# Kernel tuning notes

Measured on AMD Instinct MI355X. Metric: run time of the kernel, lower is better.

Reference implementation:

```python
import jax, jax.numpy as jnp
import numpy as np
from jax import lax

K_SIZE = 3
STRIDE = 1
PAD = 1
BN_EPS = 1e-5


def _unfold(x, k, stride, pad):
    # x: [B, C, H, W] -> patches [B, L, C*k*k] with torch.unfold feature
    # ordering (channel-major: feat = c*k*k + i*k + j), L = oH*oW
    B, C, H, W = x.shape
    xp = jnp.pad(x, ((0, 0), (0, 0), (pad, pad), (pad, pad)))
    oH = (H + 2 * pad - k) // stride + 1
    oW = (W + 2 * pad - k) // stride + 1
    views = []
    for i in range(k):
        for j in range(k):
            views.append(xp[:, :, i:i + oH * stride:stride, j:j + oW * stride:stride])
    p = jnp.stack(views, axis=0)            # [k*k, B, C, oH, oW]
    p = p.transpose(1, 3, 4, 2, 0)          # [B, oH, oW, C, k*k]
    return p.reshape(B, oH * oW, C * k * k), oH, oW


def _nearest_l1(flat, cents):
    # Online nearest-centroid search under L1, avoids [N, K] x D blowup.
    # flat: [N, D], cents: [K, D] -> int32 indices [N] (first min on ties,
    # matching torch argmin)
    N = flat.shape[0]
    init = (jnp.full((N,), jnp.inf, flat.dtype), jnp.zeros((N,), jnp.int32))
    ks = jnp.arange(cents.shape[0], dtype=jnp.int32)

    def body(carry, kc):
        kidx, c = kc
        d = jnp.abs(flat - c).sum(-1)       # [N]
        bd, bi = carry
        better = d < bd
        return (jnp.where(better, d, bd), jnp.where(better, kidx, bi)), None

    (_, best_idx), _ = lax.scan(body, init, (ks, cents))
    return best_idx


def setup_inputs() -> dict:
    key = jax.random.key(0)
    ks = jax.random.split(key, 5)
    B, Cin, H, W = 8, 64, 56, 56
    K, D, Cout = 256, Cin * K_SIZE * K_SIZE, 128
    return {
        "x": jax.random.normal(ks[0], (B, Cin, H, W), jnp.float32),
        "centroids": jax.random.normal(ks[1], (K, D), jnp.float32),
        "residual_centroids": jax.random.normal(ks[2], (K, D), jnp.float32),
        "dot_centroids": jax.random.normal(ks[3], (K, Cout), jnp.float32),
        "dot_residual_centroids": jax.random.normal(ks[4], (K, Cout), jnp.float32),
        "bn_gamma": jnp.ones((Cout,), jnp.float32),
        "bn_beta": jnp.zeros((Cout,), jnp.float32),
    }


def reference(x, centroids, residual_centroids, dot_centroids,
              dot_residual_centroids, bn_gamma, bn_beta):
    B = x.shape[0]
    Cout = dot_centroids.shape[1]
    patches, oH, oW = _unfold(x, K_SIZE, STRIDE, PAD)   # [B, L, D]
    L, D = patches.shape[1], patches.shape[2]
    flat = patches.reshape(B * L, D)

    # Stage 1: nearest centroid (L1)
    idx1 = _nearest_l1(flat, centroids)                  # [B*L]
    residuals = flat - centroids[idx1]                   # [B*L, D]
    # Stage 2: nearest residual centroid (L1)
    idx2 = _nearest_l1(residuals, residual_centroids)    # [B*L]

    # LUT gather + sum
    out_vals = dot_centroids[idx1] + dot_residual_centroids[idx2]  # [B*L, Cout]
    out = out_vals.reshape(B, L, Cout).transpose(0, 2, 1).reshape(B, Cout, oH, oW)

    # BatchNorm2d (training mode: biased batch statistics)
    mean = out.mean(axis=(0, 2, 3), keepdims=True)
    var = ((out - mean) ** 2).mean(axis=(0, 2, 3), keepdims=True)
    out = (out - mean) * lax.rsqrt(var + BN_EPS)
    out = out * bn_gamma[None, :, None, None] + bn_beta[None, :, None, None]
    return out
```

## Files before the change

### kernel.cpp

```cpp
#include <hip/hip_runtime.h>

#define NP 25088
#define DD 576
#define KC 256

__global__ __launch_bounds__(256) void unfold_kernel(const float* __restrict__ x,
                                                     float* __restrict__ PT) {
  const int d = blockIdx.y;
  const int n = blockIdx.x * 256 + threadIdx.x;
  const int c = d / 9, r = d % 9;
  const int di = r / 3 - 1, dj = r % 3 - 1;
  const int b = n / 3136, hw = n % 3136;
  const int h = hw / 56 + di, w = hw % 56 + dj;
  float v = 0.0f;
  if (h >= 0 && h < 56 && w >= 0 && w < 56)
    v = x[(((size_t)b * 64 + c) * 56 + h) * 56 + w];
  PT[(size_t)d * NP + n] = v;
}

__global__ __launch_bounds__(256) void transpose_kernel(const float* __restrict__ C,
                                                        float* __restrict__ CT) {
  const int d = blockIdx.x;
  const int k = threadIdx.x;
  CT[d * KC + k] = C[k * DD + d];
}

#define ACC4(p, a, s) \
  do { p.x += fabsf(a.x - (s)); p.y += fabsf(a.y - (s)); \
       p.z += fabsf(a.z - (s)); p.w += fabsf(a.w - (s)); } while (0)
#define ADD4(t, p) \
  do { t.x += p.x; t.y += p.y; t.z += p.z; t.w += p.w; } while (0)
#define COMP(v, i) ((i) == 0 ? (v).x : (i) == 1 ? (v).y : (i) == 2 ? (v).z : (v).w)

__global__ __launch_bounds__(256, 6) void nearest_kernel(const float* __restrict__ AT,
                                                         const float* __restrict__ CT,
                                                         float* __restrict__ distc,
                                                         int* __restrict__ idxc) {
  __shared__ float As[2][16][64];
  __shared__ float Bs[2][16][64];

  const int tid = threadIdx.x;
  const int tm = tid >> 4;
  const int tk = tid & 15;
  const int L = blockIdx.x;
  const int xcd = L & 7, r = L >> 3;
  const int mb = xcd * 49 + (r >> 2);
  const int kc = r & 3;
  const int m0 = mb * 64, k0 = kc * 64;

  float4 ra0, rb0;
  float4 p0, p1, p2, p3, t0, t1, t2, t3;

  const int frow = tid >> 4, fcol = (tid & 15) * 4;
  const float* ap = AT + (size_t)frow * NP + m0 + fcol;
  const float* bp = CT + (size_t)frow * KC + k0 + fcol;

#define LOADT() do {                                       \
    ra0 = *(const float4*)(ap);                            \
    rb0 = *(const float4*)(bp);                            \
    ap += (size_t)16 * NP; bp += 16 * KC;                  \
  } while (0)

#define WRITET(bf) do {                                    \
    *(float4*)&As[bf][frow][fcol] = ra0;                   \
    *(float4*)&Bs[bf][frow][fcol] = rb0;                   \
  } while (0)

  LOADT();
  WRITET(0);
  t0 = t1 = t2 = t3 = make_float4(0.f, 0.f, 0.f, 0.f);

  for (int ch = 0; ch < 36; ++ch) {
    if ((ch & 3) == 0) p0 = p1 = p2 = p3 = make_float4(0.f, 0.f, 0.f, 0.f);
    __syncthreads();
    if (ch < 35) LOADT();
    const float (*__restrict__ Asb)[64] = As[ch & 1];
    const float (*__restrict__ Bsb)[64] = Bs[ch & 1];
#pragma unroll 8
    for (int d = 0; d < 16; ++d) {
      const float4 a = *(const float4*)&Asb[d][tm * 4];
      const float4 b = *(const float4*)&Bsb[d][tk * 4];
      ACC4(p0, a, b.x);
      ACC4(p1, a, b.y);
      ACC4(p2, a, b.z);
      ACC4(p3, a, b.w);
    }
    if (ch < 35) WRITET((ch + 1) & 1);
    if ((ch & 3) == 3) {
      ADD4(t0, p0); ADD4(t1, p1); ADD4(t2, p2); ADD4(t3, p3);
    }
  }

#pragma unroll
  for (int i = 0; i < 4; ++i) {
    const float d0 = COMP(t0, i), d1 = COMP(t1, i), d2 = COMP(t2, i), d3 = COMP(t3, i);
    float bd = d0;
    int bk = k0 + tk * 4;
    if (d1 < bd) { bd = d1; bk = k0 + tk * 4 + 1; }
    if (d2 < bd) { bd = d2; bk = k0 + tk * 4 + 2; }
    if (d3 < bd) { bd = d3; bk = k0 + tk * 4 + 3; }
#pragma unroll
    for (int off = 1; off < 16; off <<= 1) {
      const float od = __shfl_xor(bd, off, 64);
      const int ok = __shfl_xor(bk, off, 64);
      if (od < bd || (od == bd && ok < bk)) { bd = od; bk = ok; }
    }
    if (tk == 0) {
      const int m = m0 + tm * 4 + i;
      distc[(size_t)kc * NP + m] = bd;
      idxc[(size_t)kc * NP + m] = bk;
    }
  }
#undef LOADT
#undef WRITET
}

__global__ __launch_bounds__(256) void combine_kernel(const float* __restrict__ distc,
                                                      const int* __restrict__ idxc,
                                                      int* __restrict__ idx_out) {
  const int n = blockIdx.x * 256 + threadIdx.x;
  if (n >= NP) return;
  float bd = distc[n];
  int bi = idxc[n];
#pragma unroll
  for (int s = 1; s < 4; ++s) {
    const float d = distc[(size_t)s * NP + n];
    if (d < bd) { bd = d; bi = idxc[(size_t)s * NP + n]; }
  }
  idx_out[n] = bi;
}

__global__ __launch_bounds__(256) void resid_kernel(float* __restrict__ PT,
                                                    const float* __restrict__ C1T,
                                                    const int* __restrict__ idx1) {
  const int d = blockIdx.y;
  const int n = blockIdx.x * 256 + threadIdx.x;
  const int k = idx1[n];
  PT[(size_t)d * NP + n] -= C1T[d * KC + k];
}

__global__ __launch_bounds__(256) void stats_kernel(const int* __restrict__ idx1,
                                                    const int* __restrict__ idx2,
                                                    const float* __restrict__ dotc,
                                                    const float* __restrict__ dotrc,
                                                    float* __restrict__ gsum,
                                                    float* __restrict__ gsq) {
  __shared__ float ssum[4][128], ssq[4][128];
  const int tid = threadIdx.x, lane = tid & 63, wv = tid >> 6;
  const int wid = blockIdx.x * 4 + wv;
  float s0 = 0.f, s1 = 0.f, q0 = 0.f, q1 = 0.f;
  for (int n = wid; n < NP; n += 512) {
    const int k1 = idx1[n], k2 = idx2[n];
    const float2 u = ((const float2*)(dotc + (size_t)k1 * 128))[lane];
    const float2 v = ((const float2*)(dotrc + (size_t)k2 * 128))[lane];
    const float x0 = u.x + v.x, x1 = u.y + v.y;
    s0 += x0; s1 += x1; q0 += x0 * x0; q1 += x1 * x1;
  }
  ssum[wv][lane * 2] = s0; ssum[wv][lane * 2 + 1] = s1;
  ssq[wv][lane * 2] = q0;  ssq[wv][lane * 2 + 1] = q1;
  __syncthreads();
  if (tid < 128) {
    const float s = ssum[0][tid] + ssum[1][tid] + ssum[2][tid] + ssum[3][tid];
    const float q = ssq[0][tid] + ssq[1][tid] + ssq[2][tid] + ssq[3][tid];
    atomicAdd(&gsum[tid], s);
    atomicAdd(&gsq[tid], q);
  }
}

__global__ void finalize_kernel(const float* __restrict__ gsum,
                                const float* __restrict__ gsq,
                                const float* __restrict__ gamma,
                                const float* __restrict__ beta,
                                float* __restrict__ scalev,
                                float* __restrict__ shiftv) {
  const int c = threadIdx.x;
  const float mean = gsum[c] * (1.0f / NP);
  const float var = gsq[c] * (1.0f / NP) - mean * mean;
  const float inv = rsqrtf(var + 1e-5f);
  const float sc = gamma[c] * inv;
  scalev[c] = sc;
  shiftv[c] = beta[c] - mean * sc;
}

__global__ __launch_bounds__(256) void output_kernel(const int* __restrict__ idx1,
                                                     const int* __restrict__ idx2,
                                                     const float* __restrict__ dotc,
                                                     const float* __restrict__ dotrc,
                                                     const float* __restrict__ scalev,
                                                     const float* __restrict__ shiftv,
                                                     float* __restrict__ out) {
  __shared__ float vals[64][128];
  const int tid = threadIdx.x, lane = tid & 63, wv = tid >> 6;
  const int blk = blockIdx.x;
  const int b = blk / 49, hw0 = (blk % 49) * 64;
  const int n0 = b * 3136 + hw0;
  const float sc0 = scalev[lane * 2], sc1 = scalev[lane * 2 + 1];
  const float sh0 = shiftv[lane * 2], sh1 = shiftv[lane * 2 + 1];
  for (int t = 0; t < 16; ++t) {
    const int nn = wv * 16 + t;
    const int n = n0 + nn;
    const int k1 = idx1[n], k2 = idx2[n];
    const float2 u = ((const float2*)(dotc + (size_t)k1 * 128))[lane];
    const float2 v = ((const float2*)(dotrc + (size_t)k2 * 128))[lane];
    *(float2*)&vals[nn][lane * 2] =
        make_float2(sc0 * (u.x + v.x) + sh0, sc1 * (u.y + v.y) + sh1);
  }
  __syncthreads();
  const int c = tid >> 1, half = tid & 1;
  float* op = out + ((size_t)b * 128 + c) * 3136 + hw0 + half * 32;
#pragma unroll
  for (int i = 0; i < 32; i += 4) {
    float4 w4;
    w4.x = vals[half * 32 + i + 0][c];
    w4.y = vals[half * 32 + i + 1][c];
    w4.z = vals[half * 32 + i + 2][c];
    w4.w = vals[half * 32 + i + 3][c];
    *(float4*)(op + i) = w4;
  }
}

extern "C" void kernel_launch(void* const* d_in, const int* in_sizes, int n_in,
                              void* d_out, int out_size, void* d_ws, size_t ws_size,
                              hipStream_t stream) {
  const float* x     = (const float*)d_in[0];
  const float* cent  = (const float*)d_in[1];
  const float* rcent = (const float*)d_in[2];
  const float* dotc  = (const float*)d_in[3];
  const float* dotrc = (const float*)d_in[4];
  const float* gamma = (const float*)d_in[5];
  const float* beta  = (const float*)d_in[6];
  float* out = (float*)d_out;

  float* PT  = (float*)d_ws;
  float* C1T = PT + (size_t)DD * NP;
  float* C2T = C1T + (size_t)DD * KC;
  int* idx1  = (int*)(C2T + (size_t)DD * KC);
  int* idx2  = idx1 + NP;
  float* distc = (float*)(idx2 + NP);
  int* idxc    = (int*)(distc + 4 * NP);
  float* gsum   = (float*)(idxc + 4 * NP);
  float* gsq    = gsum + 128;
  float* scalev = gsq + 128;
  float* shiftv = scalev + 128;

  unfold_kernel<<<dim3(98, 576), 256, 0, stream>>>(x, PT);
  transpose_kernel<<<576, 256, 0, stream>>>(cent, C1T);
  transpose_kernel<<<576, 256, 0, stream>>>(rcent, C2T);
  nearest_kernel<<<1568, 256, 0, stream>>>(PT, C1T, distc, idxc);
  combine_kernel<<<98, 256, 0, stream>>>(distc, idxc, idx1);
  resid_kernel<<<dim3(98, 576), 256, 0, stream>>>(PT, C1T, idx1);
  nearest_kernel<<<1568, 256, 0, stream>>>(PT, C2T, distc, idxc);
  combine_kernel<<<98, 256, 0, stream>>>(distc, idxc, idx2);
  hipMemsetAsync(gsum, 0, 256 * sizeof(float), stream);
  stats_kernel<<<128, 256, 0, stream>>>(idx1, idx2, dotc, dotrc, gsum, gsq);
  finalize_kernel<<<1, 128, 0, stream>>>(gsum, gsq, gamma, beta, scalev, shiftv);
  output_kernel<<<392, 256, 0, stream>>>(idx1, idx2, dotc, dotrc, scalev, shiftv, out);
}
```

Measured before the change: 679.4 us.

## Stage nearest-kernel tiles via direct global-to-LDS loads with deeper K chunks

The L1 nearest-centroid kernel now fills its double-buffered shared tiles with direct global-to-LDS buffer loads instead of loading into registers and storing to LDS. The per-stage depth doubles from 16 to 32 feature rows, halving the number of barriers, and the occupancy hint drops from 6 to 5 blocks per CU to fit the larger LDS footprint. This aims to save VGPRs and LDS-store instructions and to overlap the next stage's loads with compute. The risk is that the wait on the asynchronous loads before the barrier is placed correctly, and that lower occupancy hides latency less well.

```diff
diff --git a/kernel.cpp b/kernel.cpp
--- a/kernel.cpp
+++ b/kernel.cpp
@@ -1,4 +1,5 @@
 #include <hip/hip_runtime.h>
+#include <stdint.h>
 
 #define NP 25088
 #define DD 576
@@ -32,14 +33,21 @@
   do { t.x += p.x; t.y += p.y; t.z += p.z; t.w += p.w; } while (0)
 #define COMP(v, i) ((i) == 0 ? (v).x : (i) == 1 ? (v).y : (i) == 2 ? (v).z : (v).w)
 
-__global__ __launch_bounds__(256, 6) void nearest_kernel(const float* __restrict__ AT,
+__device__ __forceinline__ void gl16(const float* g, float* l) {
+  __builtin_amdgcn_global_load_lds(
+      (const __attribute__((address_space(1))) void*)(uintptr_t)g,
+      (__attribute__((address_space(3))) void*)(uintptr_t)l, 16, 0, 0);
+}
+
+__global__ __launch_bounds__(256, 5) void nearest_kernel(const float* __restrict__ AT,
                                                          const float* __restrict__ CT,
                                                          float* __restrict__ distc,
                                                          int* __restrict__ idxc) {
-  __shared__ float As[2][16][64];
-  __shared__ float Bs[2][16][64];
+  __shared__ __align__(16) float As[2][32][64];
+  __shared__ __align__(16) float Bs[2][32][64];
 
   const int tid = threadIdx.x;
+  const int lane = tid & 63, wv = tid >> 6;
   const int tm = tid >> 4;
   const int tk = tid & 15;
   const int L = blockIdx.x;
@@ -48,36 +56,31 @@
   const int kc = r & 3;
   const int m0 = mb * 64, k0 = kc * 64;
 
-  float4 ra0, rb0;
+  const int lr = lane >> 4, lc = (lane & 15) * 4;
+  const float* apg = AT + (size_t)(wv * 8 + lr) * NP + m0 + lc;
+  const float* bpg = CT + (size_t)(wv * 8 + lr) * KC + k0 + lc;
+
+#define STAGE(bf) do {                                     \
+    gl16(apg,              &As[bf][wv * 8][0]);            \
+    gl16(apg + 4 * NP,     &As[bf][wv * 8 + 4][0]);        \
+    gl16(bpg,              &Bs[bf][wv * 8][0]);            \
+    gl16(bpg + 4 * KC,     &Bs[bf][wv * 8 + 4][0]);        \
+    apg += (size_t)32 * NP; bpg += 32 * KC;                \
+  } while (0)
+
   float4 p0, p1, p2, p3, t0, t1, t2, t3;
 
-  const int frow = tid >> 4, fcol = (tid & 15) * 4;
-  const float* ap = AT + (size_t)frow * NP + m0 + fcol;
-  const float* bp = CT + (size_t)frow * KC + k0 + fcol;
-
-#define LOADT() do {                                       \
-    ra0 = *(const float4*)(ap);                            \
-    rb0 = *(const float4*)(bp);                            \
-    ap += (size_t)16 * NP; bp += 16 * KC;                  \
-  } while (0)
-
-#define WRITET(bf) do {                                    \
-    *(float4*)&As[bf][frow][fcol] = ra0;                   \
-    *(float4*)&Bs[bf][frow][fcol] = rb0;                   \
-  } while (0)
-
-  LOADT();
-  WRITET(0);
+  STAGE(0);
   t0 = t1 = t2 = t3 = make_float4(0.f, 0.f, 0.f, 0.f);
-
-  for (int ch = 0; ch < 36; ++ch) {
-    if ((ch & 3) == 0) p0 = p1 = p2 = p3 = make_float4(0.f, 0.f, 0.f, 0.f);
-    __syncthreads();
-    if (ch < 35) LOADT();
+  __syncthreads();
+
+  for (int ch = 0; ch < 18; ++ch) {
+    if ((ch & 1) == 0) p0 = p1 = p2 = p3 = make_float4(0.f, 0.f, 0.f, 0.f);
+    if (ch < 17) STAGE((ch + 1) & 1);
     const float (*__restrict__ Asb)[64] = As[ch & 1];
     const float (*__restrict__ Bsb)[64] = Bs[ch & 1];
 #pragma unroll 8
-    for (int d = 0; d < 16; ++d) {
+    for (int d = 0; d < 32; ++d) {
       const float4 a = *(const float4*)&Asb[d][tm * 4];
       const float4 b = *(const float4*)&Bsb[d][tk * 4];
       ACC4(p0, a, b.x);
@@ -85,10 +88,10 @@
       ACC4(p2, a, b.z);
       ACC4(p3, a, b.w);
     }
-    if (ch < 35) WRITET((ch + 1) & 1);
-    if ((ch & 3) == 3) {
+    if (ch & 1) {
       ADD4(t0, p0); ADD4(t1, p1); ADD4(t2, p2); ADD4(t3, p3);
     }
+    __syncthreads();
   }
 
 #pragma unroll
@@ -111,8 +114,7 @@
       idxc[(size_t)kc * NP + m] = bk;
     }
   }
-#undef LOADT
-#undef WRITET
+#undef STAGE
 }
 
 __global__ __launch_bounds__(256) void combine_kernel(const float* __restrict__ distc,
```

Result: slower. 708.8 us (+4.3%).

## Restructure L1 nearest search: one thread per centroid over row-major patches

Applied to the files above, without the earlier changes.

Patches are now stored row-major ([N, D]) rather than transposed. The nearest-centroid kernel assigns one centroid per thread and 16 points per block, with the point data read at block-uniform addresses so they can be served by scalar loads. The partial-K split, the combine kernels and the centroid transposes are removed, and the residual kernel becomes vectorized by row. The trade-off is that LDS tiling is dropped: every block re-reads the full centroid matrix through cache using strided per-thread rows, which raises L2 traffic and weakens coalescing.

```diff
diff --git a/kernel.cpp b/kernel.cpp
--- a/kernel.cpp
+++ b/kernel.cpp
@@ -1,142 +1,120 @@
 #include <hip/hip_runtime.h>
+#include <stdint.h>
 
 #define NP 25088
 #define DD 576
 #define KC 256
 
 __global__ __launch_bounds__(256) void unfold_kernel(const float* __restrict__ x,
-                                                     float* __restrict__ PT) {
-  const int d = blockIdx.y;
-  const int n = blockIdx.x * 256 + threadIdx.x;
-  const int c = d / 9, r = d % 9;
-  const int di = r / 3 - 1, dj = r % 3 - 1;
-  const int b = n / 3136, hw = n % 3136;
-  const int h = hw / 56 + di, w = hw % 56 + dj;
-  float v = 0.0f;
-  if (h >= 0 && h < 56 && w >= 0 && w < 56)
-    v = x[(((size_t)b * 64 + c) * 56 + h) * 56 + w];
-  PT[(size_t)d * NP + n] = v;
-}
-
-__global__ __launch_bounds__(256) void transpose_kernel(const float* __restrict__ C,
-                                                        float* __restrict__ CT) {
-  const int d = blockIdx.x;
-  const int k = threadIdx.x;
-  CT[d * KC + k] = C[k * DD + d];
-}
-
-#define ACC4(p, a, s) \
-  do { p.x += fabsf(a.x - (s)); p.y += fabsf(a.y - (s)); \
-       p.z += fabsf(a.z - (s)); p.w += fabsf(a.w - (s)); } while (0)
-#define ADD4(t, p) \
-  do { t.x += p.x; t.y += p.y; t.z += p.z; t.w += p.w; } while (0)
-#define COMP(v, i) ((i) == 0 ? (v).x : (i) == 1 ? (v).y : (i) == 2 ? (v).z : (v).w)
-
-__global__ __launch_bounds__(256, 6) void nearest_kernel(const float* __restrict__ AT,
-                                                         const float* __restrict__ CT,
-                                                         float* __restrict__ distc,
-                                                         int* __restrict__ idxc) {
-  __shared__ float As[2][16][64];
-  __shared__ float Bs[2][16][64];
+                                                     float* __restrict__ P) {
+  const int n0 = blockIdx.x * 16;
+#pragma unroll 1
+  for (int rr = 0; rr < 36; ++rr) {
+    const unsigned idx = rr * 256 + threadIdx.x;
+    const int n = n0 + (int)(idx / 576u);
+    const int d = (int)(idx % 576u);
+    const int c = d / 9, r = d % 9;
+    const int di = r / 3 - 1, dj = r % 3 - 1;
+    const int b = n / 3136, hw = n % 3136;
+    const int h = hw / 56 + di, w = hw % 56 + dj;
+    float v = 0.0f;
+    if (h >= 0 && h < 56 && w >= 0 && w < 56)
+      v = x[(((size_t)b * 64 + c) * 56 + h) * 56 + w];
+    P[(size_t)n * DD + d] = v;
+  }
+}
+
+#define STEP(mm, ACC) do {                                          \
+    const float* Ar_ = ap + (size_t)(mm) * DD;                      \
+    const float4 a0 = *(const float4*)(Ar_);                        \
+    const float4 a1 = *(const float4*)(Ar_ + 4);                    \
+    const float4 a2 = *(const float4*)(Ar_ + 8);                    \
+    const float4 a3 = *(const float4*)(Ar_ + 12);                   \
+    const float s_ =                                                \
+      ((((fabsf(a0.x - vb0.x) + fabsf(a0.y - vb0.y)) +              \
+         (fabsf(a0.z - vb0.z) + fabsf(a0.w - vb0.w))) +             \
+        ((fabsf(a1.x - vb1.x) + fabsf(a1.y - vb1.y)) +              \
+         (fabsf(a1.z - vb1.z) + fabsf(a1.w - vb1.w)))) +            \
+       (((fabsf(a2.x - vb2.x) + fabsf(a2.y - vb2.y)) +              \
+         (fabsf(a2.z - vb2.z) + fabsf(a2.w - vb2.w))) +             \
+        ((fabsf(a3.x - vb3.x) + fabsf(a3.y - vb3.y)) +              \
+         (fabsf(a3.z - vb3.z) + fabsf(a3.w - vb3.w)))));            \
+    ACC += s_;                                                      \
+  } while (0)
+
+#define REDUCE(mm, V) do {                                          \
+    float bd_ = (V); int bk_ = tid;                                 \
+    _Pragma("unroll")                                               \
+    for (int off_ = 1; off_ < 64; off_ <<= 1) {                     \
+      const float od_ = __shfl_xor(bd_, off_, 64);                  \
+      const int ok_ = __shfl_xor(bk_, off_, 64);                    \
+      if (od_ < bd_ || (od_ == bd_ && ok_ < bk_)) { bd_ = od_; bk_ = ok_; } \
+    }                                                               \
+    if (lane == 0) { sd[wv][mm] = bd_; si[wv][mm] = bk_; }          \
+  } while (0)
+
+__global__ __launch_bounds__(256, 4) void nearest_kernel(const float* __restrict__ A,
+                                                         const float* __restrict__ C,
+                                                         int* __restrict__ idx_out) {
+  __shared__ float sd[4][16];
+  __shared__ int si[4][16];
 
   const int tid = threadIdx.x;
-  const int tm = tid >> 4;
-  const int tk = tid & 15;
-  const int L = blockIdx.x;
-  const int xcd = L & 7, r = L >> 3;
-  const int mb = xcd * 49 + (r >> 2);
-  const int kc = r & 3;
-  const int m0 = mb * 64, k0 = kc * 64;
-
-  float4 ra0, rb0;
-  float4 p0, p1, p2, p3, t0, t1, t2, t3;
-
-  const int frow = tid >> 4, fcol = (tid & 15) * 4;
-  const float* ap = AT + (size_t)frow * NP + m0 + fcol;
-  const float* bp = CT + (size_t)frow * KC + k0 + fcol;
-
-#define LOADT() do {                                       \
-    ra0 = *(const float4*)(ap);                            \
-    rb0 = *(const float4*)(bp);                            \
-    ap += (size_t)16 * NP; bp += 16 * KC;                  \
-  } while (0)
-
-#define WRITET(bf) do {                                    \
-    *(float4*)&As[bf][frow][fcol] = ra0;                   \
-    *(float4*)&Bs[bf][frow][fcol] = rb0;                   \
-  } while (0)
-
-  LOADT();
-  WRITET(0);
-  t0 = t1 = t2 = t3 = make_float4(0.f, 0.f, 0.f, 0.f);
-
+  const int lane = tid & 63, wv = tid >> 6;
+  const int m0 = blockIdx.x * 16;
+
+  const float* ap = A + (size_t)m0 * DD;
+  const float* bp = C + (size_t)tid * DD;
+
+  float4 acc0, acc1, acc2, acc3;
+  acc0 = acc1 = acc2 = acc3 = make_float4(0.f, 0.f, 0.f, 0.f);
+
+#pragma unroll 2
   for (int ch = 0; ch < 36; ++ch) {
-    if ((ch & 3) == 0) p0 = p1 = p2 = p3 = make_float4(0.f, 0.f, 0.f, 0.f);
-    __syncthreads();
-    if (ch < 35) LOADT();
-    const float (*__restrict__ Asb)[64] = As[ch & 1];
-    const float (*__restrict__ Bsb)[64] = Bs[ch & 1];
-#pragma unroll 8
-    for (int d = 0; d < 16; ++d) {
-      const float4 a = *(const float4*)&Asb[d][tm * 4];
-      const float4 b = *(const float4*)&Bsb[d][tk * 4];
-      ACC4(p0, a, b.x);
-      ACC4(p1, a, b.y);
-      ACC4(p2, a, b.z);
-      ACC4(p3, a, b.w);
+    const float4 vb0 = *(const float4*)(bp);
+    const float4 vb1 = *(const float4*)(bp + 4);
+    const float4 vb2 = *(const float4*)(bp + 8);
+    const float4 vb3 = *(const float4*)(bp + 12);
+    STEP(0,  acc0.x); STEP(1,  acc0.y); STEP(2,  acc0.z); STEP(3,  acc0.w);
+    STEP(4,  acc1.x); STEP(5,  acc1.y); STEP(6,  acc1.z); STEP(7,  acc1.w);
+    STEP(8,  acc2.x); STEP(9,  acc2.y); STEP(10, acc2.z); STEP(11, acc2.w);
+    STEP(12, acc3.x); STEP(13, acc3.y); STEP(14, acc3.z); STEP(15, acc3.w);
+    ap += 16; bp += 16;
+  }
+
+  REDUCE(0,  acc0.x); REDUCE(1,  acc0.y); REDUCE(2,  acc0.z); REDUCE(3,  acc0.w);
+  REDUCE(4,  acc1.x); REDUCE(5,  acc1.y); REDUCE(6,  acc1.z); REDUCE(7,  acc1.w);
+  REDUCE(8,  acc2.x); REDUCE(9,  acc2.y); REDUCE(10, acc2.z); REDUCE(11, acc2.w);
+  REDUCE(12, acc3.x); REDUCE(13, acc3.y); REDUCE(14, acc3.z); REDUCE(15, acc3.w);
+
+  __syncthreads();
+  if (tid < 16) {
+    float bd = sd[0][tid];
+    int bk = si[0][tid];
+#pragma unroll
+    for (int w = 1; w < 4; ++w) {
+      const float od = sd[w][tid];
+      if (od < bd) { bd = od; bk = si[w][tid]; }
     }
-    if (ch < 35) WRITET((ch + 1) & 1);
-    if ((ch & 3) == 3) {
-      ADD4(t0, p0); ADD4(t1, p1); ADD4(t2, p2); ADD4(t3, p3);
-    }
-  }
-
-#pragma unroll
-  for (int i = 0; i < 4; ++i) {
-    const float d0 = COMP(t0, i), d1 = COMP(t1, i), d2 = COMP(t2, i), d3 = COMP(t3, i);
-    float bd = d0;
-    int bk = k0 + tk * 4;
-    if (d1 < bd) { bd = d1; bk = k0 + tk * 4 + 1; }
-    if (d2 < bd) { bd = d2; bk = k0 + tk * 4 + 2; }
-    if (d3 < bd) { bd = d3; bk = k0 + tk * 4 + 3; }
-#pragma unroll
-    for (int off = 1; off < 16; off <<= 1) {
-      const float od = __shfl_xor(bd, off, 64);
-      const int ok = __shfl_xor(bk, off, 64);
-      if (od < bd || (od == bd && ok < bk)) { bd = od; bk = ok; }
-    }
-    if (tk == 0) {
-      const int m = m0 + tm * 4 + i;
-      distc[(size_t)kc * NP + m] = bd;
-      idxc[(size_t)kc * NP + m] = bk;
-    }
-  }
-#undef LOADT
-#undef WRITET
-}
-
-__global__ __launch_bounds__(256) void combine_kernel(const float* __restrict__ distc,
-                                                      const int* __restrict__ idxc,
-                                                      int* __restrict__ idx_out) {
-  const int n = blockIdx.x * 256 + threadIdx.x;
-  if (n >= NP) return;
-  float bd = distc[n];
-  int bi = idxc[n];
-#pragma unroll
-  for (int s = 1; s < 4; ++s) {
-    const float d = distc[(size_t)s * NP + n];
-    if (d < bd) { bd = d; bi = idxc[(size_t)s * NP + n]; }
-  }
-  idx_out[n] = bi;
-}
-
-__global__ __launch_bounds__(256) void resid_kernel(float* __restrict__ PT,
-                                                    const float* __restrict__ C1T,
+    idx_out[m0 + tid] = bk;
+  }
+}
+
+__global__ __launch_bounds__(256) void resid_kernel(float* __restrict__ P,
+                                                    const float* __restrict__ C1,
                                                     const int* __restrict__ idx1) {
-  const int d = blockIdx.y;
-  const int n = blockIdx.x * 256 + threadIdx.x;
-  const int k = idx1[n];
-  PT[(size_t)d * NP + n] -= C1T[d * KC + k];
+  const int n0 = blockIdx.x * 16;
+#pragma unroll 1
+  for (int rr = 0; rr < 9; ++rr) {
+    const unsigned q = rr * 256 + threadIdx.x;
+    const int n = n0 + (int)(q / 144u);
+    const int dq = (int)(q % 144u);
+    const int k = idx1[n];
+    float4* pp = (float4*)(P + (size_t)n * DD + dq * 4);
+    const float4 pv = *pp;
+    const float4 cv = *(const float4*)(C1 + (size_t)k * DD + dq * 4);
+    *pp = make_float4(pv.x - cv.x, pv.y - cv.y, pv.z - cv.z, pv.w - cv.w);
+  }
 }
 
 __global__ __launch_bounds__(256) void stats_kernel(const int* __restrict__ idx1,
@@ -231,26 +209,18 @@
   const float* beta  = (const float*)d_in[6];
   float* out = (float*)d_out;
 
-  float* PT  = (float*)d_ws;
-  float* C1T = PT + (size_t)DD * NP;
-  float* C2T = C1T + (size_t)DD * KC;
-  int* idx1  = (int*)(C2T + (size_t)DD * KC);
+  float* P   = (float*)d_ws;
+  int* idx1  = (int*)(P + (size_t)NP * DD);
   int* idx2  = idx1 + NP;
-  float* distc = (float*)(idx2 + NP);
-  int* idxc    = (int*)(distc + 4 * NP);
-  float* gsum   = (float*)(idxc + 4 * NP);
+  float* gsum   = (float*)(idx2 + NP);
   float* gsq    = gsum + 128;
   float* scalev = gsq + 128;
   float* shiftv = scalev + 128;
 
-  unfold_kernel<<<dim3(98, 576), 256, 0, stream>>>(x, PT);
-  transpose_kernel<<<576, 256, 0, stream>>>(cent, C1T);
-  transpose_kernel<<<576, 256, 0, stream>>>(rcent, C2T);
-  nearest_kernel<<<1568, 256, 0, stream>>>(PT, C1T, distc, idxc);
-  combine_kernel<<<98, 256, 0, stream>>>(distc, idxc, idx1);
-  resid_kernel<<<dim3(98, 576), 256, 0, stream>>>(PT, C1T, idx1);
-  nearest_kernel<<<1568, 256, 0, stream>>>(PT, C2T, distc, idxc);
-  combine_kernel<<<98, 256, 0, stream>>>(distc, idxc, idx2);
+  unfold_kernel<<<1568, 256, 0, stream>>>(x, P);
+  nearest_kernel<<<1568, 256, 0, stream>>>(P, cent, idx1);
+  resid_kernel<<<1568, 256, 0, stream>>>(P, cent, idx1);
+  nearest_kernel<<<1568, 256, 0, stream>>>(P, rcent, idx2);
   hipMemsetAsync(gsum, 0, 256 * sizeof(float), stream);
   stats_kernel<<<128, 256, 0, stream>>>(idx1, idx2, dotc, dotrc, gsum, gsq);
   finalize_kernel<<<1, 128, 0, stream>>>(gsum, gsq, gamma, beta, scalev, shiftv);
```

Result: faster. 624.9 us (-8.0%).
